# Kernel optimization log

Hardware: AMD Instinct MI355X
Metric: run time of the kernel (lower is better)

Reference implementation:

```python
import jax, jax.numpy as jnp
import numpy as np
from jax import lax

DIM = 1024
INNER = 2048          # expansion * dim
GROUPS = 128          # groups in cell's 1x1 grouped convs
GSZ = INNER // GROUPS # 16
KSZ = 4               # causal conv kernel size
EPS = 1e-8


def log_g(x):
    return jnp.where(x >= 0, jnp.log(jax.nn.relu(x) + 0.5 + EPS), -jax.nn.softplus(-x) + EPS)


def setup_inputs() -> dict:
    key = jax.random.key(0)
    ks = jax.random.split(key, 10)
    B, S = 4, 4096
    std_up = float(np.sqrt(2.0 / (5 * DIM)))
    std_down = float(2.0 / 1 / np.sqrt(DIM))
    return {
        "x": jax.random.normal(ks[0], (B, S, DIM), jnp.float32),
        "w_up": jax.random.normal(ks[1], (2 * INNER, DIM), jnp.float32) * std_up,
        "b_up": jnp.zeros((2 * INNER,), jnp.float32),
        "conv_w": jax.random.normal(ks[2], (INNER, 1, KSZ), jnp.float32) * 0.25,
        "conv_b": jnp.zeros((INNER,), jnp.float32),
        "skip": jnp.ones((INNER,), jnp.float32),
        "w_f": jax.random.normal(ks[3], (GROUPS, GSZ, GSZ), jnp.float32) * 0.1,
        "w_i": jax.random.normal(ks[4], (GROUPS, GSZ, GSZ), jnp.float32) * 0.1,
        "w_h": jax.random.normal(ks[5], (GROUPS, GSZ, GSZ), jnp.float32) * 0.1,
        "w_down": jax.random.normal(ks[6], (DIM, INNER), jnp.float32) * std_down,
        "b_down": jnp.zeros((DIM,), jnp.float32),
    }


def reference(x, w_up, b_up, conv_w, conv_b, skip, w_f, w_i, w_h, w_down, b_down):
    B, S, _ = x.shape
    # proj up -> split into minlstm branch and gate branch z
    x_inner = jnp.einsum('bsd,ed->bse', x, w_up) + b_up          # (B,S,2*INNER)
    x_min, z = jnp.split(x_inner, 2, axis=-1)                    # each (B,S,INNER)

    # causal depthwise conv over time (left pad K-1, cross-correlation like torch)
    xc = lax.conv_general_dilated(
        x_min.transpose(0, 2, 1), conv_w,
        window_strides=(1,), padding=[(KSZ - 1, 0)],
        feature_group_count=INNER,
        dimension_numbers=('NCH', 'OIH', 'NCH'))
    xc = (xc + conv_b[None, :, None]).transpose(0, 2, 1)         # (B,S,INNER)
    act = jax.nn.silu(xc)

    # minLSTM cell: grouped (block-diagonal, 128 blocks of 16) 1x1 projections
    ag = act.reshape(B, S, GROUPS, GSZ)
    f_gate = jnp.einsum('bsgi,goi->bsgo', ag, w_f).reshape(B, S, INNER)
    i_gate = jnp.einsum('bsgi,goi->bsgo', ag, w_i).reshape(B, S, INNER)
    hidden = jnp.einsum('bsgi,goi->bsgo', ag, w_h).reshape(B, S, INNER)

    diff = jax.nn.softplus(-f_gate) - jax.nn.softplus(-i_gate)
    log_f = -jax.nn.softplus(diff)
    log_i = -jax.nn.softplus(-diff)
    log_tilde_h = log_g(hidden)

    # parallel log-space scan
    a_star = jnp.cumsum(log_f + EPS, axis=1)
    log_h0_b = lax.cumlogsumexp(log_i + log_tilde_h - a_star, axis=1)
    h_t = jnp.exp(a_star + log_h0_b)                             # (B,S,INNER)

    # original code keeps only last timestep of the scan, broadcast over skip path
    h = h_t[:, -1:, :] + skip * act                              # (B,S,INNER)
    h = h * jax.nn.silu(z)
    out = jnp.einsum('bse,de->bsd', h, w_down) + b_down          # (B,S,DIM)
    return out
```

## Files before the change

kernel.cpp:

```cpp
#include <hip/hip_runtime.h>
#include <math.h>

constexpr int B_  = 4;
constexpr int S_  = 4096;
constexpr int D_  = 1024;
constexpr int IN_ = 2048;
constexpr float EPS_ = 1e-8f;
constexpr int NCH_ = 128;
constexpr int CS_  = S_ / NCH_;
constexpr float LOG2E_ = 1.4426950408889634f;
constexpr float LN2_   = 0.6931471805599453f;
constexpr float EPS2_  = 1.4426950408889634e-8f;

typedef __attribute__((ext_vector_type(8))) _Float16 f16x8;
typedef __attribute__((ext_vector_type(2))) _Float16 h2;
typedef __attribute__((ext_vector_type(4))) float    f32x4;

#define BAR() asm volatile("s_barrier" ::: "memory")

__device__ __forceinline__ h2 pkrtz(float a, float b) {
  auto r = __builtin_amdgcn_cvt_pkrtz(a, b);
  union { decltype(r) r_; h2 h; } c; c.r_ = r; return c.h;
}
__device__ __forceinline__ unsigned packh2(float a, float b) {
  auto r = __builtin_amdgcn_cvt_pkrtz(a, b);
  union { decltype(r) r_; unsigned u; } c; c.r_ = r; return c.u;
}
__device__ __forceinline__ void unpack_h8(uint4 v, float* f) {
  union { uint4 u; _Float16 h[8]; } c; c.u = v;
  #pragma unroll
  for (int i = 0; i < 8; ++i) f[i] = (float)c.h[i];
}
__device__ __forceinline__ float sp2(float t) {
  const float e = __builtin_amdgcn_exp2f(-fabsf(t));
  return fmaxf(t, 0.0f) + __builtin_amdgcn_logf(1.0f + e);
}
__device__ __forceinline__ float siluf(float x) {
  return x * __builtin_amdgcn_rcpf(1.0f + __builtin_amdgcn_exp2f(-x * LOG2E_));
}

__device__ __forceinline__ void gload16(const void* g, void* l) {
  __builtin_amdgcn_global_load_lds(
      (const __attribute__((address_space(1))) void*)g,
      (__attribute__((address_space(3))) void*)l,
      16, 0, 0);
}

__launch_bounds__(256)
__global__ void cvt_f16_2(const float* __restrict__ in0, unsigned* __restrict__ out0,
                          long n8_0,
                          const float* __restrict__ in1, unsigned* __restrict__ out1,
                          long n8_1)
{
  const long total  = n8_0 + n8_1;
  const long stride = (long)gridDim.x * blockDim.x;
  for (long t = (long)blockIdx.x * blockDim.x + threadIdx.x; t < total; t += stride) {
    const float* in  = (t < n8_0) ? in0  : in1;
    unsigned*    out = (t < n8_0) ? out0 : out1;
    const long   i   = (t < n8_0) ? t    : t - n8_0;
    const float4 a = *(const float4*)(in + i * 8);
    const float4 b = *(const float4*)(in + i * 8 + 4);
    uint4 o;
    o.x = packh2(a.x, a.y);
    o.y = packh2(a.z, a.w);
    o.z = packh2(b.x, b.y);
    o.w = packh2(b.z, b.w);
    *(uint4*)(out + i * 4) = o;
  }
}

__launch_bounds__(256)
__global__ void cvt_f16(const float* __restrict__ in, unsigned* __restrict__ outp,
                        long n8)
{
  const long stride = (long)gridDim.x * blockDim.x;
  for (long i = (long)blockIdx.x * blockDim.x + threadIdx.x; i < n8; i += stride) {
    const float4 a = *(const float4*)(in + i * 8);
    const float4 b = *(const float4*)(in + i * 8 + 4);
    uint4 o;
    o.x = packh2(a.x, a.y);
    o.y = packh2(a.z, a.w);
    o.z = packh2(b.x, b.y);
    o.w = packh2(b.z, b.w);
    *(uint4*)(outp + i * 4) = o;
  }
}

template<int MODE>
__launch_bounds__(512, 2)
__global__ void gemm_mfma(const unsigned short* __restrict__ Ab,
                          const unsigned short* __restrict__ Bb,
                          const float* __restrict__ bias,
                          void* __restrict__ out0,
                          unsigned short* __restrict__ out1,
                          int M, int N, int K)
{
  constexpr int BM = 256, BN = 256, BK = 64;
  __shared__ __align__(16) unsigned short As[2][BM * BK];
  __shared__ __align__(16) unsigned short Bs[2][BN * BK];

  const int tid  = threadIdx.x;
  const int lane = tid & 63;
  const int w    = tid >> 6;
  const int wm   = w >> 2;
  const int wn   = w & 3;

  const int GX  = gridDim.x;
  const int nwg = GX * gridDim.y;
  int lin = blockIdx.y * GX + blockIdx.x;
  lin = (lin & 7) * (nwg >> 3) + (lin >> 3);
  const int m0 = (lin / GX) * BM;
  const int n0 = (lin % GX) * BN;
  const int NT = K / BK;

  const int sr   = lane >> 3;
  const int sblk = ((lane & 7) ^ sr) * 8;

  const int fr  = lane & 15;
  const int fb0 = (((lane >> 4) + 0) ^ (lane & 7)) * 8;
  const int fb1 = (((lane >> 4) + 4) ^ (lane & 7)) * 8;

  auto stage64 = [&](const unsigned short* Gp, int Kd, int grow0, int kOff,
                     unsigned short* lchunk) {
    gload16(Gp + (size_t)(grow0 + w * 8 + sr) * Kd + kOff + sblk,
            lchunk + (w * 8) * BK);
  };

  f32x4 acc[8][4] = {};

  #pragma unroll
  for (int c = 0; c < 4; ++c) stage64(Ab, K, m0 + c * 64, 0, &As[0][c * 64 * BK]);
  #pragma unroll
  for (int c = 0; c < 4; ++c) stage64(Bb, K, n0 + c * 64, 0, &Bs[0][c * 64 * BK]);
  #pragma unroll
  for (int c = 0; c < 4; ++c) stage64(Ab, K, m0 + c * 64, BK, &As[1][c * 64 * BK]);
  #pragma unroll
  for (int c = 0; c < 4; ++c) stage64(Bb, K, n0 + c * 64, BK, &Bs[1][c * 64 * BK]);
  asm volatile("s_waitcnt vmcnt(8)" ::: "memory");
  BAR();

  for (int t = 0; t < NT; ++t) {
    const int cur = t & 1;
    const unsigned short* AL = As[cur];
    const unsigned short* BL = Bs[cur];
    const int  nxtK = (t + 2) * BK;
    const bool more = (t + 2 < NT);

    f16x8 af[4][2], bf[4][2];

    #pragma unroll
    for (int i = 0; i < 4; ++i) {
      const int row = wm * 128 + i * 16 + fr;
      af[i][0] = *(const f16x8*)&AL[row * BK + fb0];
      af[i][1] = *(const f16x8*)&AL[row * BK + fb1];
    }
    #pragma unroll
    for (int j = 0; j < 2; ++j) {
      const int row = wn * 64 + j * 16 + fr;
      bf[j][0] = *(const f16x8*)&BL[row * BK + fb0];
      bf[j][1] = *(const f16x8*)&BL[row * BK + fb1];
    }
    BAR();
    __builtin_amdgcn_s_setprio(1);
    #pragma unroll
    for (int i = 0; i < 4; ++i)
      #pragma unroll
      for (int j = 0; j < 2; ++j) {
        acc[i][j] = __builtin_amdgcn_mfma_f32_16x16x32_f16(af[i][0], bf[j][0], acc[i][j], 0, 0, 0);
        acc[i][j] = __builtin_amdgcn_mfma_f32_16x16x32_f16(af[i][1], bf[j][1], acc[i][j], 0, 0, 0);
      }
    __builtin_amdgcn_s_setprio(0);
    BAR();

    #pragma unroll
    for (int j = 2; j < 4; ++j) {
      const int row = wn * 64 + j * 16 + fr;
      bf[j][0] = *(const f16x8*)&BL[row * BK + fb0];
      bf[j][1] = *(const f16x8*)&BL[row * BK + fb1];
    }
    if (more) {
      stage64(Ab, K, m0 +   0, nxtK, &As[cur][0]);
      stage64(Ab, K, m0 + 128, nxtK, &As[cur][128 * BK]);
    }
    BAR();
    __builtin_amdgcn_s_setprio(1);
    #pragma unroll
    for (int i = 0; i < 4; ++i)
      #pragma unroll
      for (int j = 2; j < 4; ++j) {
        acc[i][j] = __builtin_amdgcn_mfma_f32_16x16x32_f16(af[i][0], bf[j][0], acc[i][j], 0, 0, 0);
        acc[i][j] = __builtin_amdgcn_mfma_f32_16x16x32_f16(af[i][1], bf[j][1], acc[i][j], 0, 0, 0);
      }
    __builtin_amdgcn_s_setprio(0);
    BAR();

    #pragma unroll
    for (int i = 0; i < 4; ++i) {
      const int row = wm * 128 + 64 + i * 16 + fr;
      af[i][0] = *(const f16x8*)&AL[row * BK + fb0];
      af[i][1] = *(const f16x8*)&AL[row * BK + fb1];
    }
    if (more) {
      stage64(Bb, K, n0 +   0, nxtK, &Bs[cur][0]);
      stage64(Bb, K, n0 +  64, nxtK, &Bs[cur][64 * BK]);
    }
    BAR();
    __builtin_amdgcn_s_setprio(1);
    #pragma unroll
    for (int i = 0; i < 4; ++i)
      #pragma unroll
      for (int j = 0; j < 2; ++j) {
        acc[4 + i][j] = __builtin_amdgcn_mfma_f32_16x16x32_f16(af[i][0], bf[j][0], acc[4 + i][j], 0, 0, 0);
        acc[4 + i][j] = __builtin_amdgcn_mfma_f32_16x16x32_f16(af[i][1], bf[j][1], acc[4 + i][j], 0, 0, 0);
      }
    __builtin_amdgcn_s_setprio(0);
    BAR();

    if (more) {
      stage64(Ab, K, m0 +  64, nxtK, &As[cur][64 * BK]);
      stage64(Ab, K, m0 + 192, nxtK, &As[cur][192 * BK]);
      stage64(Bb, K, n0 + 128, nxtK, &Bs[cur][128 * BK]);
      stage64(Bb, K, n0 + 192, nxtK, &Bs[cur][192 * BK]);
    }
    BAR();
    __builtin_amdgcn_s_setprio(1);
    #pragma unroll
    for (int i = 0; i < 4; ++i)
      #pragma unroll
      for (int j = 2; j < 4; ++j) {
        acc[4 + i][j] = __builtin_amdgcn_mfma_f32_16x16x32_f16(af[i][0], bf[j][0], acc[4 + i][j], 0, 0, 0);
        acc[4 + i][j] = __builtin_amdgcn_mfma_f32_16x16x32_f16(af[i][1], bf[j][1], acc[4 + i][j], 0, 0, 0);
      }
    __builtin_amdgcn_s_setprio(0);
    if (more) asm volatile("s_waitcnt vmcnt(8)" ::: "memory");
    else      asm volatile("s_waitcnt vmcnt(0)" ::: "memory");
    BAR();
  }

  const int col = lane & 15;
  const int rb4 = (lane >> 4) * 4;

  if (MODE == 1) {
    #pragma unroll
    for (int j = 0; j < 4; ++j) {
      const int n  = n0 + wn * 64 + j * 16 + col;
      const float bv = bias[n];
      #pragma unroll
      for (int i = 0; i < 8; ++i) {
        const int mb = m0 + wm * 128 + i * 16 + rb4;
        #pragma unroll
        for (int r = 0; r < 4; ++r)
          ((float*)out0)[(size_t)(mb + r) * N + n] = acc[i][j][r] + bv;
      }
    }
  } else {
    constexpr int RS = 72;
    unsigned short* eb = (w < 4) ? ((unsigned short*)As + w * (64 * RS))
                                 : ((unsigned short*)Bs + (w - 4) * (64 * RS));
    const bool zhalf = (n0 >= IN_);
    float bv[4];
    #pragma unroll
    for (int j = 0; j < 4; ++j) bv[j] = bias[n0 + wn * 64 + j * 16 + col];

    const int lrow = lane >> 3;
    const int lc8  = (lane & 7) * 8;
    unsigned short* dst = zhalf ? out1 : (unsigned short*)out0;
    const int ncol0 = (zhalf ? n0 - IN_ : n0) + wn * 64 + lc8;

    #pragma unroll
    for (int h = 0; h < 2; ++h) {
      asm volatile("s_waitcnt lgkmcnt(0)" ::: "memory");
      #pragma unroll
      for (int i2 = 0; i2 < 4; ++i2)
        #pragma unroll
        for (int j = 0; j < 4; ++j)
          #pragma unroll
          for (int r = 0; r < 4; ++r) {
            const float v = acc[h * 4 + i2][j][r] + bv[j];
            ((_Float16*)eb)[(i2 * 16 + rb4 + r) * RS + j * 16 + col] = (_Float16)v;
          }
      asm volatile("s_waitcnt lgkmcnt(0)" ::: "memory");
      #pragma unroll
      for (int it = 0; it < 8; ++it) {
        const int row = it * 8 + lrow;
        uint4 d = *(const uint4*)&eb[row * RS + lc8];
        if (zhalf) {
          float f[8];
          unpack_h8(d, f);
          d.x = packh2(siluf(f[0]), siluf(f[1]));
          d.y = packh2(siluf(f[2]), siluf(f[3]));
          d.z = packh2(siluf(f[4]), siluf(f[5]));
          d.w = packh2(siluf(f[6]), siluf(f[7]));
        }
        const int m = m0 + wm * 128 + h * 64 + row;
        *(uint4*)(dst + (size_t)m * IN_ + ncol0) = d;
      }
    }
  }
}

__launch_bounds__(256)
__global__ void conv_silu_k(const uint4* __restrict__ xm,
                            const float* __restrict__ cw,
                            const float* __restrict__ cb,
                            uint4* __restrict__ act)
{
  const int t = blockIdx.x * 256 + threadIdx.x;
  const int c8 = t & 255;
  const int s4 = (t >> 8) & (S_ / 4 - 1);
  const int b  = t >> 18;
  const int c  = c8 * 8;
  constexpr int RW = IN_ / 8;

  float w[8][4];
  #pragma unroll
  for (int j = 0; j < 8; ++j)
    *(float4*)w[j] = *(const float4*)(cw + (size_t)(c + j) * 4);
  float bias8[8];
  *(float4*)(bias8)     = *(const float4*)(cb + c);
  *(float4*)(bias8 + 4) = *(const float4*)(cb + c + 4);

  const size_t rowb = ((size_t)b * S_ + s4 * 4) * RW + c8;
  float xf[7][8];
  #pragma unroll
  for (int i = 0; i < 7; ++i) {
    if (s4 == 0 && i < 3) {
      #pragma unroll
      for (int j = 0; j < 8; ++j) xf[i][j] = 0.0f;
    } else {
      unpack_h8(xm[rowb + (long)(i - 3) * RW], xf[i]);
    }
  }

  #pragma unroll
  for (int o = 0; o < 4; ++o) {
    float r[8];
    #pragma unroll
    for (int j = 0; j < 8; ++j) r[j] = bias8[j];
    #pragma unroll
    for (int k = 0; k < 4; ++k)
      #pragma unroll
      for (int j = 0; j < 8; ++j)
        r[j] = fmaf(xf[o + k][j], w[j][k], r[j]);
    uint4 ov;
    ov.x = packh2(siluf(r[0]), siluf(r[1]));
    ov.y = packh2(siluf(r[2]), siluf(r[3]));
    ov.z = packh2(siluf(r[4]), siluf(r[5]));
    ov.w = packh2(siluf(r[6]), siluf(r[7]));
    act[rowb + (size_t)o * RW] = ov;
  }
}

__launch_bounds__(256)
__global__ void gates_scan(const unsigned* __restrict__ actb,
                           const float* __restrict__ wf,
                           const float* __restrict__ wi,
                           const float* __restrict__ wh,
                           float2* __restrict__ part)
{
  const int T  = blockIdx.x * 256 + threadIdx.x;
  const int o  = T & 15;
  const int g  = (T >> 4) & 127;
  const int ck = (T >> 11) & (NCH_ - 1);
  const int b  = T >> 18;

  h2 Wf2[8], Wi2[8], Wh2[8];
  const float* pf = wf + ((size_t)g * 16 + o) * 16;
  const float* pi = wi + ((size_t)g * 16 + o) * 16;
  const float* ph = wh + ((size_t)g * 16 + o) * 16;
  #pragma unroll
  for (int i = 0; i < 8; ++i) {
    Wf2[i] = pkrtz(pf[2 * i] * LOG2E_, pf[2 * i + 1] * LOG2E_);
    Wi2[i] = pkrtz(pi[2 * i] * LOG2E_, pi[2 * i + 1] * LOG2E_);
    Wh2[i] = pkrtz(ph[2 * i], ph[2 * i + 1]);
  }

  float p = 0.0f, Mx = -INFINITY, Ss = 0.0f;
  const unsigned* ap = actb + ((size_t)b * S_ + (size_t)ck * CS_) * (IN_ / 2) + g * 8;
  for (int s = 0; s < CS_; ++s) {
    union { uint4 u; h2 h[4]; } A0, A1;
    A0.u = *(const uint4*)(ap);
    A1.u = *(const uint4*)(ap + 4);
    ap += IN_ / 2;
    float fg = 0.0f, ig = 0.0f, hd = 0.0f;
    #pragma unroll
    for (int i = 0; i < 4; ++i) {
      fg = __builtin_amdgcn_fdot2(A0.h[i], Wf2[i], fg, false);
      ig = __builtin_amdgcn_fdot2(A0.h[i], Wi2[i], ig, false);
      hd = __builtin_amdgcn_fdot2(A0.h[i], Wh2[i], hd, false);
    }
    #pragma unroll
    for (int i = 0; i < 4; ++i) {
      fg = __builtin_amdgcn_fdot2(A1.h[i], Wf2[i + 4], fg, false);
      ig = __builtin_amdgcn_fdot2(A1.h[i], Wi2[i + 4], ig, false);
      hd = __builtin_amdgcn_fdot2(A1.h[i], Wh2[i + 4], hd, false);
    }
    const float diff  = sp2(-fg) - sp2(-ig);
    const float log_f = -sp2(diff);
    const float log_i = diff + log_f;
    const float lpos  = __builtin_amdgcn_logf(hd + 0.5f + EPS_);
    const float lneg  = -sp2(-hd * LOG2E_) + EPS2_;
    const float log_th = (hd >= 0.0f) ? lpos : lneg;
    p += log_f + EPS2_;
    const float v = log_i + log_th - p;
    const float m = fmaxf(Mx, v);
    Ss = Ss * __builtin_amdgcn_exp2f(Mx - m) + __builtin_amdgcn_exp2f(v - m);
    Mx = m;
  }
  part[((size_t)(b * IN_ + g * 16 + o)) * NCH_ + ck] =
      make_float2(p, Mx + __builtin_amdgcn_logf(Ss));
}

__launch_bounds__(256)
__global__ void combine_k(const float2* __restrict__ part, float* __restrict__ hlast)
{
  const int seq = blockIdx.x * 256 + threadIdx.x;
  if (seq >= B_ * IN_) return;
  const float2* pp = part + (size_t)seq * NCH_;
  float P = 0.0f, Mx = -INFINITY, Ss = 0.0f;
  for (int c = 0; c < NCH_; ++c) {
    const float2 al = pp[c];
    const float v = al.y - P;
    const float m = fmaxf(Mx, v);
    Ss = Ss * __builtin_amdgcn_exp2f(Mx - m) + __builtin_amdgcn_exp2f(v - m);
    Mx = m;
    P += al.x;
  }
  hlast[seq] = __builtin_amdgcn_exp2f(P + Mx) * Ss;
}

__launch_bounds__(256)
__global__ void gfuse_k(const unsigned* __restrict__ actb,
                        unsigned* __restrict__ zb,
                        const float* __restrict__ hlast,
                        const float* __restrict__ skipv)
{
  const size_t total  = (size_t)B_ * S_ * IN_ / 8;
  const size_t stride = (size_t)gridDim.x * blockDim.x;
  for (size_t t = (size_t)blockIdx.x * blockDim.x + threadIdx.x; t < total; t += stride) {
    const size_t e = t * 8;
    const int    c = (int)(e % IN_);
    const int    b = (int)(e / ((size_t)S_ * IN_));
    float a[8], z[8], hl[8], sk[8];
    unpack_h8(*(const uint4*)(actb + e / 2), a);
    unpack_h8(*(const uint4*)(zb   + e / 2), z);
    *(float4*)(hl)     = *(const float4*)(hlast + (size_t)b * IN_ + c);
    *(float4*)(hl + 4) = *(const float4*)(hlast + (size_t)b * IN_ + c + 4);
    *(float4*)(sk)     = *(const float4*)(skipv + c);
    *(float4*)(sk + 4) = *(const float4*)(skipv + c + 4);
    float g[8];
    #pragma unroll
    for (int j = 0; j < 8; ++j) g[j] = (hl[j] + sk[j] * a[j]) * z[j];
    uint4 o;
    o.x = packh2(g[0], g[1]);
    o.y = packh2(g[2], g[3]);
    o.z = packh2(g[4], g[5]);
    o.w = packh2(g[6], g[7]);
    *(uint4*)(zb + e / 2) = o;
  }
}

extern "C" void kernel_launch(void* const* d_in, const int* in_sizes, int n_in,
                              void* d_out, int out_size, void* d_ws, size_t ws_size,
                              hipStream_t stream)
{
  const float* x     = (const float*)d_in[0];
  const float* w_up  = (const float*)d_in[1];
  const float* b_up  = (const float*)d_in[2];
  const float* cw    = (const float*)d_in[3];
  const float* cb    = (const float*)d_in[4];
  const float* skipv = (const float*)d_in[5];
  const float* w_f   = (const float*)d_in[6];
  const float* w_i   = (const float*)d_in[7];
  const float* w_h   = (const float*)d_in[8];
  const float* w_dn  = (const float*)d_in[9];
  const float* b_dn  = (const float*)d_in[10];
  float* out = (float*)d_out;

  char* ws = (char*)d_ws;
  unsigned short* xminb = (unsigned short*)(ws);
  unsigned short* wdb   = (unsigned short*)(ws);
  float2*         part  = (float2*)(ws + 8388608ULL);
  float*          hlast = (float*)(ws + 16777216ULL);
  unsigned short* zb    = (unsigned short*)(ws + 67108864ULL);
  unsigned short* actb  = (unsigned short*)(ws + 134217728ULL);
  unsigned short* xb    = (unsigned short*)(ws + 134217728ULL);
  unsigned short* wub   = (unsigned short*)(ws + 201326592ULL);

  const int M = B_ * S_;

  cvt_f16_2<<<2560, 256, 0, stream>>>(
      x,    (unsigned*)xb,  (long)M * D_ / 8,
      w_up, (unsigned*)wub, (long)2 * IN_ * D_ / 8);

  gemm_mfma<0><<<dim3((2 * IN_) / 256, M / 256), 512, 0, stream>>>(
      xb, wub, b_up, xminb, (unsigned short*)zb, M, 2 * IN_, D_);

  conv_silu_k<<<(B_ * (S_ / 4) * (IN_ / 8)) / 256, 256, 0, stream>>>(
      (const uint4*)xminb, cw, cb, (uint4*)actb);

  cvt_f16<<<256, 256, 0, stream>>>(w_dn, (unsigned*)wdb, (long)D_ * IN_ / 8);

  gates_scan<<<(B_ * 128 * 16 * NCH_) / 256, 256, 0, stream>>>(
      (const unsigned*)actb, w_f, w_i, w_h, part);

  combine_k<<<(B_ * IN_ + 255) / 256, 256, 0, stream>>>(part, hlast);

  gfuse_k<<<2048, 256, 0, stream>>>((const unsigned*)actb, (unsigned*)zb, hlast, skipv);

  gemm_mfma<1><<<dim3(D_ / 256, M / 256), 512, 0, stream>>>(
      zb, wdb, b_dn, out, nullptr, M, D_, IN_);
}
```

Baseline: 398.1 us.

## Restructure GEMM to 128x256x32 tiles with triple-buffered LDS pipeline

Shrinks the GEMM block tile from 256x256x64 to 128x256x32 and replaces the double-buffered, four-phase interleaved loop with a simpler triple-buffered ring where stage t+2 loads are issued before computing stage t. It raises the occupancy hint to 4 waves-per-EU blocks, doubles the grid along M, and adapts the epilogue to 32-row chunks. The intent is more blocks in flight and better latency hiding. The cost is lower per-block arithmetic intensity, more global traffic, and one barrier per short K=32 step.

```diff
diff --git a/kernel.cpp b/kernel.cpp
--- a/kernel.cpp
+++ b/kernel.cpp
@@ -87,7 +87,7 @@
 }
 
 template<int MODE>
-__launch_bounds__(512, 2)
+__launch_bounds__(512, 4)
 __global__ void gemm_mfma(const unsigned short* __restrict__ Ab,
                           const unsigned short* __restrict__ Bb,
                           const float* __restrict__ bias,
@@ -95,9 +95,8 @@
                           unsigned short* __restrict__ out1,
                           int M, int N, int K)
 {
-  constexpr int BM = 256, BN = 256, BK = 64;
-  __shared__ __align__(16) unsigned short As[2][BM * BK];
-  __shared__ __align__(16) unsigned short Bs[2][BN * BK];
+  constexpr int BM = 128, BN = 256, BK = 32;
+  __shared__ __align__(16) unsigned short Ls[3 * BM * BK + 3 * BN * BK];
 
   const int tid  = threadIdx.x;
   const int lane = tid & 63;
@@ -113,128 +112,61 @@
   const int n0 = (lin % GX) * BN;
   const int NT = K / BK;
 
-  const int sr   = lane >> 3;
-  const int sblk = ((lane & 7) ^ sr) * 8;
+  const int sr2  = lane >> 2;
+  const int sblk = ((lane & 3) ^ ((lane >> 3) & 3)) * 8;
 
   const int fr  = lane & 15;
-  const int fb0 = (((lane >> 4) + 0) ^ (lane & 7)) * 8;
-  const int fb1 = (((lane >> 4) + 4) ^ (lane & 7)) * 8;
-
-  auto stage64 = [&](const unsigned short* Gp, int Kd, int grow0, int kOff,
-                     unsigned short* lchunk) {
-    gload16(Gp + (size_t)(grow0 + w * 8 + sr) * Kd + kOff + sblk,
-            lchunk + (w * 8) * BK);
+  const int fcb = (((lane >> 4) ^ ((lane >> 1) & 3))) * 8;
+
+  auto stageA = [&](int buf, int kOff) {
+    gload16(Ab + (size_t)(m0 + w * 16 + sr2) * K + kOff + sblk,
+            &Ls[buf * (BM * BK) + (w * 16) * BK]);
   };
-
-  f32x4 acc[8][4] = {};
-
-  #pragma unroll
-  for (int c = 0; c < 4; ++c) stage64(Ab, K, m0 + c * 64, 0, &As[0][c * 64 * BK]);
-  #pragma unroll
-  for (int c = 0; c < 4; ++c) stage64(Bb, K, n0 + c * 64, 0, &Bs[0][c * 64 * BK]);
-  #pragma unroll
-  for (int c = 0; c < 4; ++c) stage64(Ab, K, m0 + c * 64, BK, &As[1][c * 64 * BK]);
-  #pragma unroll
-  for (int c = 0; c < 4; ++c) stage64(Bb, K, n0 + c * 64, BK, &Bs[1][c * 64 * BK]);
-  asm volatile("s_waitcnt vmcnt(8)" ::: "memory");
+  auto stageB = [&](int buf, int kOff) {
+    gload16(Bb + (size_t)(n0 + w * 16 + sr2) * K + kOff + sblk,
+            &Ls[3 * BM * BK + buf * (BN * BK) + (w * 16) * BK]);
+    gload16(Bb + (size_t)(n0 + 128 + w * 16 + sr2) * K + kOff + sblk,
+            &Ls[3 * BM * BK + buf * (BN * BK) + (128 + w * 16) * BK]);
+  };
+
+  f32x4 acc[4][4] = {};
+
+  stageA(0, 0);  stageB(0, 0);
+  stageA(1, BK); stageB(1, BK);
+  asm volatile("s_waitcnt vmcnt(3)" ::: "memory");
   BAR();
 
+  int bufc = 0;
   for (int t = 0; t < NT; ++t) {
-    const int cur = t & 1;
-    const unsigned short* AL = As[cur];
-    const unsigned short* BL = Bs[cur];
-    const int  nxtK = (t + 2) * BK;
-    const bool more = (t + 2 < NT);
-
-    f16x8 af[4][2], bf[4][2];
-
-    #pragma unroll
-    for (int i = 0; i < 4; ++i) {
-      const int row = wm * 128 + i * 16 + fr;
-      af[i][0] = *(const f16x8*)&AL[row * BK + fb0];
-      af[i][1] = *(const f16x8*)&AL[row * BK + fb1];
-    }
-    #pragma unroll
-    for (int j = 0; j < 2; ++j) {
-      const int row = wn * 64 + j * 16 + fr;
-      bf[j][0] = *(const f16x8*)&BL[row * BK + fb0];
-      bf[j][1] = *(const f16x8*)&BL[row * BK + fb1];
-    }
+    const unsigned short* AL = &Ls[bufc * (BM * BK)];
+    const unsigned short* BL = &Ls[3 * BM * BK + bufc * (BN * BK)];
+    const int bufn = (bufc + 2 >= 3) ? bufc - 1 : bufc + 2;
+
+    if (t + 2 < NT) {
+      stageA(bufn, (t + 2) * BK);
+      stageB(bufn, (t + 2) * BK);
+    }
+
+    f16x8 af[4], bf[4];
+    #pragma unroll
+    for (int i = 0; i < 4; ++i)
+      af[i] = *(const f16x8*)&AL[(wm * 64 + i * 16 + fr) * BK + fcb];
+    #pragma unroll
+    for (int j = 0; j < 4; ++j)
+      bf[j] = *(const f16x8*)&BL[(wn * 64 + j * 16 + fr) * BK + fcb];
+
     BAR();
     __builtin_amdgcn_s_setprio(1);
     #pragma unroll
     for (int i = 0; i < 4; ++i)
       #pragma unroll
-      for (int j = 0; j < 2; ++j) {
-        acc[i][j] = __builtin_amdgcn_mfma_f32_16x16x32_f16(af[i][0], bf[j][0], acc[i][j], 0, 0, 0);
-        acc[i][j] = __builtin_amdgcn_mfma_f32_16x16x32_f16(af[i][1], bf[j][1], acc[i][j], 0, 0, 0);
-      }
+      for (int j = 0; j < 4; ++j)
+        acc[i][j] = __builtin_amdgcn_mfma_f32_16x16x32_f16(af[i], bf[j], acc[i][j], 0, 0, 0);
     __builtin_amdgcn_s_setprio(0);
+    if (t + 2 < NT) asm volatile("s_waitcnt vmcnt(3)" ::: "memory");
+    else            asm volatile("s_waitcnt vmcnt(0)" ::: "memory");
     BAR();
-
-    #pragma unroll
-    for (int j = 2; j < 4; ++j) {
-      const int row = wn * 64 + j * 16 + fr;
-      bf[j][0] = *(const f16x8*)&BL[row * BK + fb0];
-      bf[j][1] = *(const f16x8*)&BL[row * BK + fb1];
-    }
-    if (more) {
-      stage64(Ab, K, m0 +   0, nxtK, &As[cur][0]);
-      stage64(Ab, K, m0 + 128, nxtK, &As[cur][128 * BK]);
-    }
-    BAR();
-    __builtin_amdgcn_s_setprio(1);
-    #pragma unroll
-    for (int i = 0; i < 4; ++i)
-      #pragma unroll
-      for (int j = 2; j < 4; ++j) {
-        acc[i][j] = __builtin_amdgcn_mfma_f32_16x16x32_f16(af[i][0], bf[j][0], acc[i][j], 0, 0, 0);
-        acc[i][j] = __builtin_amdgcn_mfma_f32_16x16x32_f16(af[i][1], bf[j][1], acc[i][j], 0, 0, 0);
-      }
-    __builtin_amdgcn_s_setprio(0);
-    BAR();
-
-    #pragma unroll
-    for (int i = 0; i < 4; ++i) {
-      const int row = wm * 128 + 64 + i * 16 + fr;
-      af[i][0] = *(const f16x8*)&AL[row * BK + fb0];
-      af[i][1] = *(const f16x8*)&AL[row * BK + fb1];
-    }
-    if (more) {
-      stage64(Bb, K, n0 +   0, nxtK, &Bs[cur][0]);
-      stage64(Bb, K, n0 +  64, nxtK, &Bs[cur][64 * BK]);
-    }
-    BAR();
-    __builtin_amdgcn_s_setprio(1);
-    #pragma unroll
-    for (int i = 0; i < 4; ++i)
-      #pragma unroll
-      for (int j = 0; j < 2; ++j) {
-        acc[4 + i][j] = __builtin_amdgcn_mfma_f32_16x16x32_f16(af[i][0], bf[j][0], acc[4 + i][j], 0, 0, 0);
-        acc[4 + i][j] = __builtin_amdgcn_mfma_f32_16x16x32_f16(af[i][1], bf[j][1], acc[4 + i][j], 0, 0, 0);
-      }
-    __builtin_amdgcn_s_setprio(0);
-    BAR();
-
-    if (more) {
-      stage64(Ab, K, m0 +  64, nxtK, &As[cur][64 * BK]);
-      stage64(Ab, K, m0 + 192, nxtK, &As[cur][192 * BK]);
-      stage64(Bb, K, n0 + 128, nxtK, &Bs[cur][128 * BK]);
-      stage64(Bb, K, n0 + 192, nxtK, &Bs[cur][192 * BK]);
-    }
-    BAR();
-    __builtin_amdgcn_s_setprio(1);
-    #pragma unroll
-    for (int i = 0; i < 4; ++i)
-      #pragma unroll
-      for (int j = 2; j < 4; ++j) {
-        acc[4 + i][j] = __builtin_amdgcn_mfma_f32_16x16x32_f16(af[i][0], bf[j][0], acc[4 + i][j], 0, 0, 0);
-        acc[4 + i][j] = __builtin_amdgcn_mfma_f32_16x16x32_f16(af[i][1], bf[j][1], acc[4 + i][j], 0, 0, 0);
-      }
-    __builtin_amdgcn_s_setprio(0);
-    if (more) asm volatile("s_waitcnt vmcnt(8)" ::: "memory");
-    else      asm volatile("s_waitcnt vmcnt(0)" ::: "memory");
-    BAR();
+    bufc = (bufc + 1 >= 3) ? 0 : bufc + 1;
   }
 
   const int col = lane & 15;
@@ -246,17 +178,17 @@
       const int n  = n0 + wn * 64 + j * 16 + col;
       const float bv = bias[n];
       #pragma unroll
-      for (int i = 0; i < 8; ++i) {
-        const int mb = m0 + wm * 128 + i * 16 + rb4;
+      for (int i = 0; i < 4; ++i) {
+        const int mb = m0 + wm * 64 + i * 16 + rb4;
         #pragma unroll
         for (int r = 0; r < 4; ++r)
           ((float*)out0)[(size_t)(mb + r) * N + n] = acc[i][j][r] + bv;
       }
     }
   } else {
+    BAR();
     constexpr int RS = 72;
-    unsigned short* eb = (w < 4) ? ((unsigned short*)As + w * (64 * RS))
-                                 : ((unsigned short*)Bs + (w - 4) * (64 * RS));
+    unsigned short* eb = Ls + w * (32 * RS);
     const bool zhalf = (n0 >= IN_);
     float bv[4];
     #pragma unroll
@@ -268,20 +200,20 @@
     const int ncol0 = (zhalf ? n0 - IN_ : n0) + wn * 64 + lc8;
 
     #pragma unroll
-    for (int h = 0; h < 2; ++h) {
+    for (int p = 0; p < 2; ++p) {
       asm volatile("s_waitcnt lgkmcnt(0)" ::: "memory");
       #pragma unroll
-      for (int i2 = 0; i2 < 4; ++i2)
+      for (int i2 = 0; i2 < 2; ++i2)
         #pragma unroll
         for (int j = 0; j < 4; ++j)
           #pragma unroll
           for (int r = 0; r < 4; ++r) {
-            const float v = acc[h * 4 + i2][j][r] + bv[j];
+            const float v = acc[p * 2 + i2][j][r] + bv[j];
             ((_Float16*)eb)[(i2 * 16 + rb4 + r) * RS + j * 16 + col] = (_Float16)v;
           }
       asm volatile("s_waitcnt lgkmcnt(0)" ::: "memory");
       #pragma unroll
-      for (int it = 0; it < 8; ++it) {
+      for (int it = 0; it < 4; ++it) {
         const int row = it * 8 + lrow;
         uint4 d = *(const uint4*)&eb[row * RS + lc8];
         if (zhalf) {
@@ -292,7 +224,7 @@
           d.z = packh2(siluf(f[4]), siluf(f[5]));
           d.w = packh2(siluf(f[6]), siluf(f[7]));
         }
-        const int m = m0 + wm * 128 + h * 64 + row;
+        const int m = m0 + wm * 64 + p * 32 + row;
         *(uint4*)(dst + (size_t)m * IN_ + ncol0) = d;
       }
     }
@@ -493,7 +425,7 @@
       x,    (unsigned*)xb,  (long)M * D_ / 8,
       w_up, (unsigned*)wub, (long)2 * IN_ * D_ / 8);
 
-  gemm_mfma<0><<<dim3((2 * IN_) / 256, M / 256), 512, 0, stream>>>(
+  gemm_mfma<0><<<dim3((2 * IN_) / 256, M / 128), 512, 0, stream>>>(
       xb, wub, b_up, xminb, (unsigned short*)zb, M, 2 * IN_, D_);
 
   conv_silu_k<<<(B_ * (S_ / 4) * (IN_ / 8)) / 256, 256, 0, stream>>>(
@@ -508,6 +440,6 @@
 
   gfuse_k<<<2048, 256, 0, stream>>>((const unsigned*)actb, (unsigned*)zb, hlast, skipv);
 
-  gemm_mfma<1><<<dim3(D_ / 256, M / 256), 512, 0, stream>>>(
+  gemm_mfma<1><<<dim3(D_ / 256, M / 128), 512, 0, stream>>>(
       zb, wdb, b_dn, out, nullptr, M, D_, IN_);
 }
```

After: 420.5 us. 5.7% more time.
